# Performance work log

Measured on AMD Instinct MI355X. Metric: run time of the kernel, lower is better.

Reference implementation:

```python
import jax, jax.numpy as jnp
import numpy as np
import math

N = 1024
C = 128
H = 4
HD = C // H  # 32
HID = C // 2  # geom_mlp hidden


def setup_inputs() -> dict:
    key = jax.random.key(0)
    ks = jax.random.split(key, 12)
    s = 0.02
    return {
        "x": jax.random.normal(ks[0], (N, C), jnp.float32),
        "y": jax.random.normal(ks[1], (N, C), jnp.float32),
        "pos": jax.random.normal(ks[2], (N, 3), jnp.float32),
        "Wq": jax.random.normal(ks[3], (C, C), jnp.float32) * s,
        "bq": jnp.zeros((C,), jnp.float32),
        "Wk": jax.random.normal(ks[4], (C, C), jnp.float32) * s,
        "bk": jnp.zeros((C,), jnp.float32),
        "Wv": jax.random.normal(ks[5], (C, C), jnp.float32) * s,
        "bv": jnp.zeros((C,), jnp.float32),
        "W1": jax.random.normal(ks[6], (3, HID), jnp.float32) * s,
        "b1": jnp.zeros((HID,), jnp.float32),
        "W2": jax.random.normal(ks[7], (HID, C), jnp.float32) * s,
        "b2": jnp.zeros((C,), jnp.float32),
    }


def _safe_norm(sq):
    # sqrt with zero (sub)gradient at 0, matching torch.norm behavior
    pos_mask = sq > 0
    return jnp.where(pos_mask, jnp.sqrt(jnp.where(pos_mask, sq, 1.0)), 0.0)


def reference(x, y, pos, Wq, bq, Wk, bk, Wv, bv, W1, b1, W2, b2):
    # pairwise geometry
    pos_diff = pos[:, None, :] - pos[None, :, :]          # [N, N, 3]
    dist = _safe_norm(jnp.sum(pos_diff * pos_diff, -1))   # [N, N]
    geom = jax.nn.relu(pos_diff @ W1 + b1) @ W2 + b2      # [N, N, C]
    geom = geom.reshape(N, N, H, HD)                      # per-head split

    q = (x @ Wq + bq).reshape(N, H, HD)
    k = (y @ Wk + bk).reshape(N, H, HD)
    v = (y @ Wv + bv).reshape(N, H, HD)

    attn = jnp.einsum("ihd,jhd->hij", q, k) / math.sqrt(HD)  # [H, N, N]
    geom_attn = jnp.einsum("ihd,ijhd->hij", q, geom)         # [H, N, N]
    scores = attn + geom_attn - dist[None, :, :]
    p = jax.nn.softmax(scores, axis=-1)
    out = jnp.einsum("hij,jhd->ihd", p, v).reshape(N, C)     # [N, C]
    return out
```

## Files before the change

### kernel.cpp

```cpp
#include <hip/hip_runtime.h>
#include <math.h>


typedef float v2f __attribute__((ext_vector_type(2)));
typedef float v4f __attribute__((ext_vector_type(4)));

#define L2E 1.4426950408889634f
#define RSL (0.17677669529663687f * L2E)

static __device__ __forceinline__ float dot4(float4 a, float4 b) {
  return a.x*b.x + a.y*b.y + a.z*b.z + a.w*b.w;
}
static __device__ __forceinline__ v2f fma2(v2f a, v2f b, v2f c) {
  return __builtin_elementwise_fma(a, b, c);
}
static __device__ __forceinline__ v4f fma4s(float s, v4f b, v4f c) {
  v4f sv = {s, s, s, s};
  return __builtin_elementwise_fma(sv, b, c);
}
static __device__ __forceinline__ unsigned int bfr(float f) {
  unsigned int b = __float_as_uint(f);
  return (b + 0x7fffu + ((b >> 16) & 1u)) >> 16;
}
static __device__ __forceinline__ unsigned int pack2(float lo, float hi) {
  return bfr(lo) | (bfr(hi) << 16);
}
static __device__ __forceinline__ v2f unpk(unsigned int a) {
  v2f r;
  r.x = __uint_as_float(a << 16);
  r.y = __uint_as_float(a & 0xffff0000u);
  return r;
}

__global__ __launch_bounds__(384) void k_pre(
    const float* __restrict__ x, const float* __restrict__ y, const float* __restrict__ pos,
    const float* __restrict__ Wq, const float* __restrict__ bq,
    const float* __restrict__ Wk, const float* __restrict__ bk,
    const float* __restrict__ Wv, const float* __restrict__ bv,
    const float* __restrict__ W1, const float* __restrict__ b1,
    const float* __restrict__ W2, const float* __restrict__ b2,
    float* __restrict__ q, float* __restrict__ v,
    unsigned int* __restrict__ kTb, unsigned int* __restrict__ uTb,
    float* __restrict__ sA, float* __restrict__ pos4w)
{
  __shared__ float xs[256], ys[256], qs[256];
  __shared__ __align__(16) float4 W2S[64*33];

  const int t  = threadIdx.x;
  const int n0 = blockIdx.x * 2;

  if (t < 256) { xs[t] = x[n0*128 + t]; ys[t] = y[n0*128 + t]; }
  {
    const float4* w2g = (const float4*)W2;
    #pragma unroll
    for (int r = 0; r < 6; ++r) {
      const int e = t + 384*r;
      if (e < 2048) W2S[(e>>5)*33 + (e&31)] = w2g[e];
    }
  }
  __syncthreads();

  {
    const int c   = t & 127;
    const int mat = t >> 7;
    const float* W    = (mat == 0) ? Wq : (mat == 1 ? Wk : Wv);
    const float* S    = (mat == 0) ? xs : ys;
    const float* bias = (mat == 0) ? bq : (mat == 1 ? bk : bv);
    float a0 = 0.f, a1 = 0.f;
    #pragma unroll 8
    for (int d = 0; d < 128; ++d) {
      const float w_ = W[d*128 + c];
      a0 = fmaf(S[d],       w_, a0);
      a1 = fmaf(S[128 + d], w_, a1);
    }
    const float bb = bias[c];
    a0 += bb; a1 += bb;
    if (mat == 0) {
      q[n0*128 + c] = a0 * RSL; q[(n0+1)*128 + c] = a1 * RSL;
      qs[c] = a0; qs[128 + c] = a1;
    } else if (mat == 2) {
      v[n0*128 + c] = a0; v[(n0+1)*128 + c] = a1;
    } else {
      const float b0 = __shfl_xor(a0, 1);
      const float b1 = __shfl_xor(a1, 1);
      if ((c & 1) == 0) {
        const int idx = ((c>>2)*1024)*2 + ((c>>1)&1);
        kTb[idx + (n0  )*2] = pack2(a0, b0);
        kTb[idx + (n0+1)*2] = pack2(a1, b1);
      }
    }
  }
  __syncthreads();

  if (t < 256) {
    const int m = t & 63, h = t >> 6;
    const float4* qs4 = (const float4*)qs;
    #pragma unroll
    for (int ii = 0; ii < 2; ++ii) {
      float acc = 0.f;
      #pragma unroll
      for (int ch = 0; ch < 8; ++ch)
        acc += dot4(qs4[ii*32 + h*8 + ch], W2S[m*33 + h*8 + ch]);
      sA[(n0+ii)*328 + 8 + (m>>2)*20 + h*4 + (m&3)] = acc * L2E;
    }
    if (t < 8) {
      const int ii = t >> 2, h2 = t & 3;
      float ca = 0.f;
      #pragma unroll
      for (int d = 0; d < 32; ++d) ca = fmaf(qs[ii*128 + h2*32 + d], b2[h2*32 + d], ca);
      sA[(n0+ii)*328 + h2] = ca * L2E;
    } else if (t < 16) {
      const int tt = t-8, ii = tt>>2, cc = tt&3;
      sA[(n0+ii)*328 + 4 + cc] = (cc < 3) ? pos[(n0+ii)*3 + cc] * L2E : 0.f;
    } else if (t < 24) {
      const int tt = t-16, ii = tt>>2, cc = tt&3;
      pos4w[(n0+ii)*4 + cc] = (cc < 3) ? pos[(n0+ii)*3 + cc] * L2E : 0.f;
    }
  } else if (t < 320) {
    const int tt = t - 256, ii = tt >> 5, mp = tt & 31;
    const int m0 = mp * 2;
    float ua0 = 0.f, ua1 = 0.f;
    #pragma unroll
    for (int cc = 0; cc < 3; ++cc) {
      const float p = pos[(n0+ii)*3 + cc];
      ua0 = fmaf(p, W1[cc*64 + m0    ], ua0);
      ua1 = fmaf(p, W1[cc*64 + m0 + 1], ua1);
    }
    sA[(n0+ii)*328 + 8 + (m0>>2)*20 + 16 + (m0&3)    ] = ua0 + b1[m0];
    sA[(n0+ii)*328 + 8 + (m0>>2)*20 + 16 + (m0&3) + 1] = ua1 + b1[m0+1];
    uTb[((mp>>1)*1024 + (n0+ii))*2 + (mp&1)] = pack2(ua0, ua1);
  }
}

__global__ __launch_bounds__(1024, 8) void k_attn(
    const float* __restrict__ q, const float* __restrict__ v,
    const uint2* __restrict__ kTb, const uint2* __restrict__ uTb,
    const float* __restrict__ sA, const v4f* __restrict__ pos4,
    float* __restrict__ out)
{
  __shared__ __align__(16) float eL[16*544];
  __shared__ __align__(16) float rnum[8192];
  __shared__ float rden[128];

  const int t     = threadIdx.x;
  const int i0    = blockIdx.x * 2;
  const int w     = t >> 6;
  const int lane  = t & 63;
  const int c4    = lane & 31;
  const int rep   = lane >> 5;
  const int hh    = c4 >> 3;

  const int jb = w*64;
  const int j  = jb + lane;

  const float* sA0 = sA + i0*328;
  const float* sA1 = sA0 + 328;
  const float* q0  = q + i0*128;
  const float* q1  = q0 + 128;

  const float c00 = sA0[0], c01 = sA0[1], c02 = sA0[2], c03 = sA0[3];
  const float c10 = sA1[0], c11 = sA1[1], c12 = sA1[2], c13 = sA1[3];
  const float p0x = sA0[4], p0y = sA0[5], p0z = sA0[6];
  const float p1x = sA1[4], p1y = sA1[5], p1z = sA1[6];

  const v4f pj = pos4[j];
  const float d0x = p0x-pj.x, d0y = p0y-pj.y, d0z = p0z-pj.z;
  const float d1x = p1x-pj.x, d1y = p1y-pj.y, d1z = p1z-pj.z;
  const float dist0 = sqrtf(d0x*d0x + d0y*d0y + d0z*d0z);
  const float dist1 = sqrtf(d1x*d1x + d1y*d1y + d1z*d1z);

  v2f g0a={0.f,0.f}, g0b={0.f,0.f}, g0c={0.f,0.f}, g0d={0.f,0.f};
  v2f g1a={0.f,0.f}, g1b={0.f,0.f}, g1c={0.f,0.f}, g1d={0.f,0.f};
  #pragma unroll 4
  for (int mb = 0; mb < 16; ++mb) {
    const uint2 up_ = uTb[mb*1024 + j];
    const v2f uj01 = unpk(up_.x), uj23 = unpk(up_.y);
    const v2f z = {0.f, 0.f};
    {
      const float* ab = sA0 + 8 + mb*20;
      const v2f h01 = __builtin_elementwise_max(*(const v2f*)(ab+16) - uj01, z);
      const v2f h23 = __builtin_elementwise_max(*(const v2f*)(ab+18) - uj23, z);
      g0a = fma2(h01, *(const v2f*)(ab+ 0), g0a); g0a = fma2(h23, *(const v2f*)(ab+ 2), g0a);
      g0b = fma2(h01, *(const v2f*)(ab+ 4), g0b); g0b = fma2(h23, *(const v2f*)(ab+ 6), g0b);
      g0c = fma2(h01, *(const v2f*)(ab+ 8), g0c); g0c = fma2(h23, *(const v2f*)(ab+10), g0c);
      g0d = fma2(h01, *(const v2f*)(ab+12), g0d); g0d = fma2(h23, *(const v2f*)(ab+14), g0d);
    }
    {
      const float* ab = sA1 + 8 + mb*20;
      const v2f h01 = __builtin_elementwise_max(*(const v2f*)(ab+16) - uj01, z);
      const v2f h23 = __builtin_elementwise_max(*(const v2f*)(ab+18) - uj23, z);
      g1a = fma2(h01, *(const v2f*)(ab+ 0), g1a); g1a = fma2(h23, *(const v2f*)(ab+ 2), g1a);
      g1b = fma2(h01, *(const v2f*)(ab+ 4), g1b); g1b = fma2(h23, *(const v2f*)(ab+ 6), g1b);
      g1c = fma2(h01, *(const v2f*)(ab+ 8), g1c); g1c = fma2(h23, *(const v2f*)(ab+10), g1c);
      g1d = fma2(h01, *(const v2f*)(ab+12), g1d); g1d = fma2(h23, *(const v2f*)(ab+14), g1d);
    }
  }

  v2f s0a={0.f,0.f}, s0b={0.f,0.f}, s0c={0.f,0.f}, s0d={0.f,0.f};
  v2f s1a={0.f,0.f}, s1b={0.f,0.f}, s1c={0.f,0.f}, s1d={0.f,0.f};
  #pragma unroll 8
  for (int cb = 0; cb < 8; ++cb) {
    const uint2 kp0 = kTb[(cb     )*1024 + j];
    const uint2 kp1 = kTb[(cb +  8)*1024 + j];
    const uint2 kp2 = kTb[(cb + 16)*1024 + j];
    const uint2 kp3 = kTb[(cb + 24)*1024 + j];
    const v2f k0a = unpk(kp0.x), k0b = unpk(kp0.y);
    const v2f k1a = unpk(kp1.x), k1b = unpk(kp1.y);
    const v2f k2a = unpk(kp2.x), k2b = unpk(kp2.y);
    const v2f k3a = unpk(kp3.x), k3b = unpk(kp3.y);
    s0a = fma2(k0a, *(const v2f*)(q0 + cb*4      ), s0a); s0a = fma2(k0b, *(const v2f*)(q0 + cb*4 +  2), s0a);
    s0b = fma2(k1a, *(const v2f*)(q0 + cb*4 + 32 ), s0b); s0b = fma2(k1b, *(const v2f*)(q0 + cb*4 + 34), s0b);
    s0c = fma2(k2a, *(const v2f*)(q0 + cb*4 + 64 ), s0c); s0c = fma2(k2b, *(const v2f*)(q0 + cb*4 + 66), s0c);
    s0d = fma2(k3a, *(const v2f*)(q0 + cb*4 + 96 ), s0d); s0d = fma2(k3b, *(const v2f*)(q0 + cb*4 + 98), s0d);
    s1a = fma2(k0a, *(const v2f*)(q1 + cb*4      ), s1a); s1a = fma2(k0b, *(const v2f*)(q1 + cb*4 +  2), s1a);
    s1b = fma2(k1a, *(const v2f*)(q1 + cb*4 + 32 ), s1b); s1b = fma2(k1b, *(const v2f*)(q1 + cb*4 + 34), s1b);
    s1c = fma2(k2a, *(const v2f*)(q1 + cb*4 + 64 ), s1c); s1c = fma2(k2b, *(const v2f*)(q1 + cb*4 + 66), s1c);
    s1d = fma2(k3a, *(const v2f*)(q1 + cb*4 + 96 ), s1d); s1d = fma2(k3b, *(const v2f*)(q1 + cb*4 + 98), s1d);
  }

  float lsum[8];
  float* eW = &eL[w*544];
  {
    const v2f t0a = s0a + g0a, t0b = s0b + g0b, t0c = s0c + g0c, t0d = s0d + g0d;
    const float p0 = exp2f(t0a.x + t0a.y + (c00 - dist0));
    const float p1 = exp2f(t0b.x + t0b.y + (c01 - dist0));
    const float p2 = exp2f(t0c.x + t0c.y + (c02 - dist0));
    const float p3 = exp2f(t0d.x + t0d.y + (c03 - dist0));
    lsum[0] = p0; lsum[1] = p1; lsum[2] = p2; lsum[3] = p3;
    eW[      lane] = p0; eW[ 68 + lane] = p1; eW[136 + lane] = p2; eW[204 + lane] = p3;
    const v2f t1a = s1a + g1a, t1b = s1b + g1b, t1c = s1c + g1c, t1d = s1d + g1d;
    const float r0 = exp2f(t1a.x + t1a.y + (c10 - dist1));
    const float r1 = exp2f(t1b.x + t1b.y + (c11 - dist1));
    const float r2 = exp2f(t1c.x + t1c.y + (c12 - dist1));
    const float r3 = exp2f(t1d.x + t1d.y + (c13 - dist1));
    lsum[4] = r0; lsum[5] = r1; lsum[6] = r2; lsum[7] = r3;
    eW[272 + lane] = r0; eW[340 + lane] = r1; eW[408 + lane] = r2; eW[476 + lane] = r3;
  }
  __builtin_amdgcn_wave_barrier();

  v4f acc0 = {0.f,0.f,0.f,0.f};
  v4f acc1 = {0.f,0.f,0.f,0.f};
  {
    const v4f* er0 = (const v4f*)&eL[w*544 +  hh    *68 + rep*32];
    const v4f* er1 = (const v4f*)&eL[w*544 + (4+hh) *68 + rep*32];
    const v4f* vg = (const v4f*)(v + jb*128);
    const int vbase = rep*32*32 + c4;
    #pragma unroll 4
    for (int jj4 = 0; jj4 < 8; ++jj4) {
      const v4f e0 = er0[jj4];
      const v4f e1 = er1[jj4];
      const v4f va = vg[vbase + (jj4*4+0)*32];
      const v4f vb = vg[vbase + (jj4*4+1)*32];
      const v4f vc = vg[vbase + (jj4*4+2)*32];
      const v4f vd = vg[vbase + (jj4*4+3)*32];
      acc0 = fma4s(e0.x, va, acc0); acc1 = fma4s(e1.x, va, acc1);
      acc0 = fma4s(e0.y, vb, acc0); acc1 = fma4s(e1.y, vb, acc1);
      acc0 = fma4s(e0.z, vc, acc0); acc1 = fma4s(e1.z, vc, acc1);
      acc0 = fma4s(e0.w, vd, acc0); acc1 = fma4s(e1.w, vd, acc1);
    }
  }
  __builtin_amdgcn_wave_barrier();

  #pragma unroll
  for (int mm = 1; mm < 64; mm <<= 1) {
    #pragma unroll
    for (int r8 = 0; r8 < 8; ++r8) lsum[r8] += __shfl_xor(lsum[r8], mm);
  }
  ((v4f*)rnum)[((w*2+0)*2 + rep)*32 + c4] = acc0;
  ((v4f*)rnum)[((w*2+1)*2 + rep)*32 + c4] = acc1;
  if (lane == 0) {
    #pragma unroll
    for (int r8 = 0; r8 < 8; ++r8) rden[w*8 + r8] = lsum[r8];
  }
  __syncthreads();

  if (t < 256) {
    const int ii = t >> 7, c = t & 127;
    float num = 0.f, den = 0.f;
    #pragma unroll
    for (int ww = 0; ww < 16; ++ww) {
      num += rnum[((ww*2+ii)*2+0)*128 + c];
      num += rnum[((ww*2+ii)*2+1)*128 + c];
      den += rden[ww*8 + ii*4 + (c>>5)];
    }
    out[(i0+ii)*128 + c] = num / den;
  }
}

extern "C" void kernel_launch(void* const* d_in, const int* in_sizes, int n_in,
                              void* d_out, int out_size, void* d_ws, size_t ws_size,
                              hipStream_t stream) {
  const float* x   = (const float*)d_in[0];
  const float* y   = (const float*)d_in[1];
  const float* pos = (const float*)d_in[2];
  const float* Wq  = (const float*)d_in[3];
  const float* bq  = (const float*)d_in[4];
  const float* Wk  = (const float*)d_in[5];
  const float* bk  = (const float*)d_in[6];
  const float* Wv  = (const float*)d_in[7];
  const float* bv  = (const float*)d_in[8];
  const float* W1  = (const float*)d_in[9];
  const float* b1  = (const float*)d_in[10];
  const float* W2  = (const float*)d_in[11];
  const float* b2  = (const float*)d_in[12];

  float* ws = (float*)d_ws;
  float*        q    = ws;
  float*        v    = ws + 131072;
  unsigned int* kTb  = (unsigned int*)(ws + 262144);
  unsigned int* uTb  = (unsigned int*)(ws + 327680);
  float*        sA   = ws + 360448;
  float*        pos4 = ws + 696320;
  float*        out  = (float*)d_out;

  k_pre<<<dim3(512), dim3(384), 0, stream>>>(x, y, pos, Wq, bq, Wk, bk, Wv, bv,
                                             W1, b1, W2, b2,
                                             q, v, kTb, uTb, sA, pos4);
  k_attn<<<dim3(512), dim3(1024), 0, stream>>>(q, v, (const uint2*)kTb,
                                               (const uint2*)uTb, sA,
                                               (const v4f*)pos4, out);
}
```

Baseline: 116.9 us.

## Process four query rows per attention block to reuse K, U and V loads

Each k_attn block now handles four query rows instead of two, which halves the grid to 256 blocks. Every j-column load of uTb, kTb, pos4 and V is shared across four rows, so per-row global and L1 traffic is lower. Geometry and QK partial sums now go into a single accumulator set per row, and the lsum reduction is moved ahead of the PV loop. In exchange, register pressure and LDS usage double, launch bounds drop to four blocks per CU, and 256 blocks may underfill a 256-CU device.

```diff
diff --git a/kernel.cpp b/kernel.cpp
--- a/kernel.cpp
+++ b/kernel.cpp
@@ -132,18 +132,18 @@
   }
 }
 
-__global__ __launch_bounds__(1024, 8) void k_attn(
+__global__ __launch_bounds__(1024, 4) void k_attn(
     const float* __restrict__ q, const float* __restrict__ v,
     const uint2* __restrict__ kTb, const uint2* __restrict__ uTb,
     const float* __restrict__ sA, const v4f* __restrict__ pos4,
     float* __restrict__ out)
 {
-  __shared__ __align__(16) float eL[16*544];
-  __shared__ __align__(16) float rnum[8192];
-  __shared__ float rden[128];
+  __shared__ __align__(16) float eL[16*1088];
+  __shared__ __align__(16) float rnum[16384];
+  __shared__ float rden[256];
 
   const int t     = threadIdx.x;
-  const int i0    = blockIdx.x * 2;
+  const int i0    = blockIdx.x * 4;
   const int w     = t >> 6;
   const int lane  = t & 63;
   const int c4    = lane & 31;
@@ -155,50 +155,63 @@
 
   const float* sA0 = sA + i0*328;
   const float* sA1 = sA0 + 328;
+  const float* sA2 = sA0 + 656;
+  const float* sA3 = sA0 + 984;
   const float* q0  = q + i0*128;
   const float* q1  = q0 + 128;
+  const float* q2  = q0 + 256;
+  const float* q3  = q0 + 384;
 
   const float c00 = sA0[0], c01 = sA0[1], c02 = sA0[2], c03 = sA0[3];
   const float c10 = sA1[0], c11 = sA1[1], c12 = sA1[2], c13 = sA1[3];
+  const float c20 = sA2[0], c21 = sA2[1], c22 = sA2[2], c23 = sA2[3];
+  const float c30 = sA3[0], c31 = sA3[1], c32 = sA3[2], c33 = sA3[3];
   const float p0x = sA0[4], p0y = sA0[5], p0z = sA0[6];
   const float p1x = sA1[4], p1y = sA1[5], p1z = sA1[6];
+  const float p2x = sA2[4], p2y = sA2[5], p2z = sA2[6];
+  const float p3x = sA3[4], p3y = sA3[5], p3z = sA3[6];
 
   const v4f pj = pos4[j];
   const float d0x = p0x-pj.x, d0y = p0y-pj.y, d0z = p0z-pj.z;
   const float d1x = p1x-pj.x, d1y = p1y-pj.y, d1z = p1z-pj.z;
+  const float d2x = p2x-pj.x, d2y = p2y-pj.y, d2z = p2z-pj.z;
+  const float d3x = p3x-pj.x, d3y = p3y-pj.y, d3z = p3z-pj.z;
   const float dist0 = sqrtf(d0x*d0x + d0y*d0y + d0z*d0z);
   const float dist1 = sqrtf(d1x*d1x + d1y*d1y + d1z*d1z);
-
-  v2f g0a={0.f,0.f}, g0b={0.f,0.f}, g0c={0.f,0.f}, g0d={0.f,0.f};
-  v2f g1a={0.f,0.f}, g1b={0.f,0.f}, g1c={0.f,0.f}, g1d={0.f,0.f};
-  #pragma unroll 4
+  const float dist2 = sqrtf(d2x*d2x + d2y*d2y + d2z*d2z);
+  const float dist3 = sqrtf(d3x*d3x + d3y*d3y + d3z*d3z);
+
+  v2f s0a={0.f,0.f}, s0b={0.f,0.f}, s0c={0.f,0.f}, s0d={0.f,0.f};
+  v2f s1a={0.f,0.f}, s1b={0.f,0.f}, s1c={0.f,0.f}, s1d={0.f,0.f};
+  v2f s2a={0.f,0.f}, s2b={0.f,0.f}, s2c={0.f,0.f}, s2d={0.f,0.f};
+  v2f s3a={0.f,0.f}, s3b={0.f,0.f}, s3c={0.f,0.f}, s3d={0.f,0.f};
+  const v2f z = {0.f, 0.f};
+
+#define GEOM_ROW(r) { \
+    const float* ab = sA##r + 8 + mb*20; \
+    const v2f h01 = __builtin_elementwise_max(*(const v2f*)(ab+16) - uj01, z); \
+    const v2f h23 = __builtin_elementwise_max(*(const v2f*)(ab+18) - uj23, z); \
+    s##r##a = fma2(h01, *(const v2f*)(ab+ 0), s##r##a); s##r##a = fma2(h23, *(const v2f*)(ab+ 2), s##r##a); \
+    s##r##b = fma2(h01, *(const v2f*)(ab+ 4), s##r##b); s##r##b = fma2(h23, *(const v2f*)(ab+ 6), s##r##b); \
+    s##r##c = fma2(h01, *(const v2f*)(ab+ 8), s##r##c); s##r##c = fma2(h23, *(const v2f*)(ab+10), s##r##c); \
+    s##r##d = fma2(h01, *(const v2f*)(ab+12), s##r##d); s##r##d = fma2(h23, *(const v2f*)(ab+14), s##r##d); \
+  }
+  #pragma unroll 2
   for (int mb = 0; mb < 16; ++mb) {
     const uint2 up_ = uTb[mb*1024 + j];
     const v2f uj01 = unpk(up_.x), uj23 = unpk(up_.y);
-    const v2f z = {0.f, 0.f};
-    {
-      const float* ab = sA0 + 8 + mb*20;
-      const v2f h01 = __builtin_elementwise_max(*(const v2f*)(ab+16) - uj01, z);
-      const v2f h23 = __builtin_elementwise_max(*(const v2f*)(ab+18) - uj23, z);
-      g0a = fma2(h01, *(const v2f*)(ab+ 0), g0a); g0a = fma2(h23, *(const v2f*)(ab+ 2), g0a);
-      g0b = fma2(h01, *(const v2f*)(ab+ 4), g0b); g0b = fma2(h23, *(const v2f*)(ab+ 6), g0b);
-      g0c = fma2(h01, *(const v2f*)(ab+ 8), g0c); g0c = fma2(h23, *(const v2f*)(ab+10), g0c);
-      g0d = fma2(h01, *(const v2f*)(ab+12), g0d); g0d = fma2(h23, *(const v2f*)(ab+14), g0d);
-    }
-    {
-      const float* ab = sA1 + 8 + mb*20;
-      const v2f h01 = __builtin_elementwise_max(*(const v2f*)(ab+16) - uj01, z);
-      const v2f h23 = __builtin_elementwise_max(*(const v2f*)(ab+18) - uj23, z);
-      g1a = fma2(h01, *(const v2f*)(ab+ 0), g1a); g1a = fma2(h23, *(const v2f*)(ab+ 2), g1a);
-      g1b = fma2(h01, *(const v2f*)(ab+ 4), g1b); g1b = fma2(h23, *(const v2f*)(ab+ 6), g1b);
-      g1c = fma2(h01, *(const v2f*)(ab+ 8), g1c); g1c = fma2(h23, *(const v2f*)(ab+10), g1c);
-      g1d = fma2(h01, *(const v2f*)(ab+12), g1d); g1d = fma2(h23, *(const v2f*)(ab+14), g1d);
-    }
-  }
-
-  v2f s0a={0.f,0.f}, s0b={0.f,0.f}, s0c={0.f,0.f}, s0d={0.f,0.f};
-  v2f s1a={0.f,0.f}, s1b={0.f,0.f}, s1c={0.f,0.f}, s1d={0.f,0.f};
-  #pragma unroll 8
+    GEOM_ROW(0) GEOM_ROW(1) GEOM_ROW(2) GEOM_ROW(3)
+  }
+#undef GEOM_ROW
+
+#define QK_ROW(r) { \
+    const float* qq = q##r + cb*4; \
+    s##r##a = fma2(k0a, *(const v2f*)(qq      ), s##r##a); s##r##a = fma2(k0b, *(const v2f*)(qq +  2), s##r##a); \
+    s##r##b = fma2(k1a, *(const v2f*)(qq + 32 ), s##r##b); s##r##b = fma2(k1b, *(const v2f*)(qq + 34), s##r##b); \
+    s##r##c = fma2(k2a, *(const v2f*)(qq + 64 ), s##r##c); s##r##c = fma2(k2b, *(const v2f*)(qq + 66), s##r##c); \
+    s##r##d = fma2(k3a, *(const v2f*)(qq + 96 ), s##r##d); s##r##d = fma2(k3b, *(const v2f*)(qq + 98), s##r##d); \
+  }
+  #pragma unroll 2
   for (int cb = 0; cb < 8; ++cb) {
     const uint2 kp0 = kTb[(cb     )*1024 + j];
     const uint2 kp1 = kTb[(cb +  8)*1024 + j];
@@ -208,80 +221,85 @@
     const v2f k1a = unpk(kp1.x), k1b = unpk(kp1.y);
     const v2f k2a = unpk(kp2.x), k2b = unpk(kp2.y);
     const v2f k3a = unpk(kp3.x), k3b = unpk(kp3.y);
-    s0a = fma2(k0a, *(const v2f*)(q0 + cb*4      ), s0a); s0a = fma2(k0b, *(const v2f*)(q0 + cb*4 +  2), s0a);
-    s0b = fma2(k1a, *(const v2f*)(q0 + cb*4 + 32 ), s0b); s0b = fma2(k1b, *(const v2f*)(q0 + cb*4 + 34), s0b);
-    s0c = fma2(k2a, *(const v2f*)(q0 + cb*4 + 64 ), s0c); s0c = fma2(k2b, *(const v2f*)(q0 + cb*4 + 66), s0c);
-    s0d = fma2(k3a, *(const v2f*)(q0 + cb*4 + 96 ), s0d); s0d = fma2(k3b, *(const v2f*)(q0 + cb*4 + 98), s0d);
-    s1a = fma2(k0a, *(const v2f*)(q1 + cb*4      ), s1a); s1a = fma2(k0b, *(const v2f*)(q1 + cb*4 +  2), s1a);
-    s1b = fma2(k1a, *(const v2f*)(q1 + cb*4 + 32 ), s1b); s1b = fma2(k1b, *(const v2f*)(q1 + cb*4 + 34), s1b);
-    s1c = fma2(k2a, *(const v2f*)(q1 + cb*4 + 64 ), s1c); s1c = fma2(k2b, *(const v2f*)(q1 + cb*4 + 66), s1c);
-    s1d = fma2(k3a, *(const v2f*)(q1 + cb*4 + 96 ), s1d); s1d = fma2(k3b, *(const v2f*)(q1 + cb*4 + 98), s1d);
-  }
-
-  float lsum[8];
-  float* eW = &eL[w*544];
-  {
-    const v2f t0a = s0a + g0a, t0b = s0b + g0b, t0c = s0c + g0c, t0d = s0d + g0d;
-    const float p0 = exp2f(t0a.x + t0a.y + (c00 - dist0));
-    const float p1 = exp2f(t0b.x + t0b.y + (c01 - dist0));
-    const float p2 = exp2f(t0c.x + t0c.y + (c02 - dist0));
-    const float p3 = exp2f(t0d.x + t0d.y + (c03 - dist0));
-    lsum[0] = p0; lsum[1] = p1; lsum[2] = p2; lsum[3] = p3;
-    eW[      lane] = p0; eW[ 68 + lane] = p1; eW[136 + lane] = p2; eW[204 + lane] = p3;
-    const v2f t1a = s1a + g1a, t1b = s1b + g1b, t1c = s1c + g1c, t1d = s1d + g1d;
-    const float r0 = exp2f(t1a.x + t1a.y + (c10 - dist1));
-    const float r1 = exp2f(t1b.x + t1b.y + (c11 - dist1));
-    const float r2 = exp2f(t1c.x + t1c.y + (c12 - dist1));
-    const float r3 = exp2f(t1d.x + t1d.y + (c13 - dist1));
-    lsum[4] = r0; lsum[5] = r1; lsum[6] = r2; lsum[7] = r3;
-    eW[272 + lane] = r0; eW[340 + lane] = r1; eW[408 + lane] = r2; eW[476 + lane] = r3;
-  }
+    QK_ROW(0) QK_ROW(1) QK_ROW(2) QK_ROW(3)
+  }
+#undef QK_ROW
+
+  float lsum[16];
+  float* eW = &eL[w*1088];
+#define EXP_ROW(r, C0, C1, C2, C3, DIST) { \
+    const float p0 = exp2f(s##r##a.x + s##r##a.y + (C0 - DIST)); \
+    const float p1 = exp2f(s##r##b.x + s##r##b.y + (C1 - DIST)); \
+    const float p2 = exp2f(s##r##c.x + s##r##c.y + (C2 - DIST)); \
+    const float p3 = exp2f(s##r##d.x + s##r##d.y + (C3 - DIST)); \
+    lsum[r*4+0] = p0; lsum[r*4+1] = p1; lsum[r*4+2] = p2; lsum[r*4+3] = p3; \
+    eW[(r*4+0)*68 + lane] = p0; eW[(r*4+1)*68 + lane] = p1; \
+    eW[(r*4+2)*68 + lane] = p2; eW[(r*4+3)*68 + lane] = p3; \
+  }
+  EXP_ROW(0, c00, c01, c02, c03, dist0)
+  EXP_ROW(1, c10, c11, c12, c13, dist1)
+  EXP_ROW(2, c20, c21, c22, c23, dist2)
+  EXP_ROW(3, c30, c31, c32, c33, dist3)
+#undef EXP_ROW
   __builtin_amdgcn_wave_barrier();
+
+  #pragma unroll
+  for (int mm = 1; mm < 64; mm <<= 1) {
+    #pragma unroll
+    for (int r16 = 0; r16 < 16; ++r16) lsum[r16] += __shfl_xor(lsum[r16], mm);
+  }
+  if (lane == 0) {
+    #pragma unroll
+    for (int r16 = 0; r16 < 16; ++r16) rden[w*16 + r16] = lsum[r16];
+  }
 
   v4f acc0 = {0.f,0.f,0.f,0.f};
   v4f acc1 = {0.f,0.f,0.f,0.f};
+  v4f acc2 = {0.f,0.f,0.f,0.f};
+  v4f acc3 = {0.f,0.f,0.f,0.f};
   {
-    const v4f* er0 = (const v4f*)&eL[w*544 +  hh    *68 + rep*32];
-    const v4f* er1 = (const v4f*)&eL[w*544 + (4+hh) *68 + rep*32];
+    const v4f* er0 = (const v4f*)&eL[w*1088 + ( 0 + hh)*68 + rep*32];
+    const v4f* er1 = (const v4f*)&eL[w*1088 + ( 4 + hh)*68 + rep*32];
+    const v4f* er2 = (const v4f*)&eL[w*1088 + ( 8 + hh)*68 + rep*32];
+    const v4f* er3 = (const v4f*)&eL[w*1088 + (12 + hh)*68 + rep*32];
     const v4f* vg = (const v4f*)(v + jb*128);
     const int vbase = rep*32*32 + c4;
-    #pragma unroll 4
+    #pragma unroll 2
     for (int jj4 = 0; jj4 < 8; ++jj4) {
       const v4f e0 = er0[jj4];
       const v4f e1 = er1[jj4];
+      const v4f e2 = er2[jj4];
+      const v4f e3 = er3[jj4];
       const v4f va = vg[vbase + (jj4*4+0)*32];
       const v4f vb = vg[vbase + (jj4*4+1)*32];
       const v4f vc = vg[vbase + (jj4*4+2)*32];
       const v4f vd = vg[vbase + (jj4*4+3)*32];
       acc0 = fma4s(e0.x, va, acc0); acc1 = fma4s(e1.x, va, acc1);
+      acc2 = fma4s(e2.x, va, acc2); acc3 = fma4s(e3.x, va, acc3);
       acc0 = fma4s(e0.y, vb, acc0); acc1 = fma4s(e1.y, vb, acc1);
+      acc2 = fma4s(e2.y, vb, acc2); acc3 = fma4s(e3.y, vb, acc3);
       acc0 = fma4s(e0.z, vc, acc0); acc1 = fma4s(e1.z, vc, acc1);
+      acc2 = fma4s(e2.z, vc, acc2); acc3 = fma4s(e3.z, vc, acc3);
       acc0 = fma4s(e0.w, vd, acc0); acc1 = fma4s(e1.w, vd, acc1);
+      acc2 = fma4s(e2.w, vd, acc2); acc3 = fma4s(e3.w, vd, acc3);
     }
   }
   __builtin_amdgcn_wave_barrier();
 
-  #pragma unroll
-  for (int mm = 1; mm < 64; mm <<= 1) {
-    #pragma unroll
-    for (int r8 = 0; r8 < 8; ++r8) lsum[r8] += __shfl_xor(lsum[r8], mm);
-  }
-  ((v4f*)rnum)[((w*2+0)*2 + rep)*32 + c4] = acc0;
-  ((v4f*)rnum)[((w*2+1)*2 + rep)*32 + c4] = acc1;
-  if (lane == 0) {
-    #pragma unroll
-    for (int r8 = 0; r8 < 8; ++r8) rden[w*8 + r8] = lsum[r8];
-  }
+  ((v4f*)rnum)[((w*4+0)*2 + rep)*32 + c4] = acc0;
+  ((v4f*)rnum)[((w*4+1)*2 + rep)*32 + c4] = acc1;
+  ((v4f*)rnum)[((w*4+2)*2 + rep)*32 + c4] = acc2;
+  ((v4f*)rnum)[((w*4+3)*2 + rep)*32 + c4] = acc3;
   __syncthreads();
 
-  if (t < 256) {
+  if (t < 512) {
     const int ii = t >> 7, c = t & 127;
     float num = 0.f, den = 0.f;
     #pragma unroll
     for (int ww = 0; ww < 16; ++ww) {
-      num += rnum[((ww*2+ii)*2+0)*128 + c];
-      num += rnum[((ww*2+ii)*2+1)*128 + c];
-      den += rden[ww*8 + ii*4 + (c>>5)];
+      num += rnum[((ww*4+ii)*2+0)*128 + c];
+      num += rnum[((ww*4+ii)*2+1)*128 + c];
+      den += rden[ww*16 + ii*4 + (c>>5)];
     }
     out[(i0+ii)*128 + c] = num / den;
   }
@@ -316,7 +334,7 @@
   k_pre<<<dim3(512), dim3(384), 0, stream>>>(x, y, pos, Wq, bq, Wk, bk, Wv, bv,
                                              W1, b1, W2, b2,
                                              q, v, kTb, uTb, sA, pos4);
-  k_attn<<<dim3(512), dim3(1024), 0, stream>>>(q, v, (const uint2*)kTb,
+  k_attn<<<dim3(256), dim3(1024), 0, stream>>>(q, v, (const uint2*)kTb,
                                                (const uint2*)uTb, sA,
                                                (const v4f*)pos4, out);
 }
```

Measured after the change: 120.4 us. +3.0%, slower.

## Switch QK and PV products to packed fp16 dot2 with repacked layouts

Applied to the files above, without the earlier changes.

Stores q, k and v as packed fp16 pairs in new layouts (k as 8-word rows, v interleaved across j pairs, u widened to 4-word loads) and computes both the QK scores and the P·V accumulation with v_dot2 fp16 instructions. Probabilities are rounded to fp16, packed two per word in LDS, and the denominator is built from the same rounded values so it stays consistent with the numerator. This halves LDS and global traffic for e and v and reduces the FMA count. In exchange it loses precision (fp16 range and rounding for q, k, v and p) and adds extra shuffles for packing.

```diff
diff --git a/kernel.cpp b/kernel.cpp
--- a/kernel.cpp
+++ b/kernel.cpp
@@ -1,9 +1,11 @@
 #include <hip/hip_runtime.h>
+#include <hip/hip_fp16.h>
 #include <math.h>
 
 
 typedef float v2f __attribute__((ext_vector_type(2)));
 typedef float v4f __attribute__((ext_vector_type(4)));
+typedef __fp16 h2f __attribute__((ext_vector_type(2)));
 
 #define L2E 1.4426950408889634f
 #define RSL (0.17677669529663687f * L2E)
@@ -13,10 +15,6 @@
 }
 static __device__ __forceinline__ v2f fma2(v2f a, v2f b, v2f c) {
   return __builtin_elementwise_fma(a, b, c);
-}
-static __device__ __forceinline__ v4f fma4s(float s, v4f b, v4f c) {
-  v4f sv = {s, s, s, s};
-  return __builtin_elementwise_fma(sv, b, c);
 }
 static __device__ __forceinline__ unsigned int bfr(float f) {
   unsigned int b = __float_as_uint(f);
@@ -30,6 +28,24 @@
   r.x = __uint_as_float(a << 16);
   r.y = __uint_as_float(a & 0xffff0000u);
   return r;
+}
+static __device__ __forceinline__ unsigned int pkh(float lo, float hi) {
+  h2f r = __builtin_amdgcn_cvt_pkrtz(lo, hi);
+  return __builtin_bit_cast(unsigned int, r);
+}
+static __device__ __forceinline__ unsigned int pkrn(float lo, float hi) {
+  unsigned int a = (unsigned int)__half_as_ushort(__float2half(lo));
+  unsigned int b = (unsigned int)__half_as_ushort(__float2half(hi));
+  return a | (b << 16);
+}
+static __device__ __forceinline__ float fdot2h(unsigned int a_, unsigned int b_, float acc) {
+  return __builtin_amdgcn_fdot2(__builtin_bit_cast(h2f, a_),
+                                __builtin_bit_cast(h2f, b_), acc, false);
+}
+static __device__ __forceinline__ float r2h(float x, unsigned int* bits) {
+  h2f t = __builtin_amdgcn_cvt_pkrtz(x, x);
+  *bits = __builtin_bit_cast(unsigned int, t) & 0xffffu;
+  return (float)t.x;
 }
 
 __global__ __launch_bounds__(384) void k_pre(
@@ -39,8 +55,8 @@
     const float* __restrict__ Wv, const float* __restrict__ bv,
     const float* __restrict__ W1, const float* __restrict__ b1,
     const float* __restrict__ W2, const float* __restrict__ b2,
-    float* __restrict__ q, float* __restrict__ v,
-    unsigned int* __restrict__ kTb, unsigned int* __restrict__ uTb,
+    unsigned int* __restrict__ qT, unsigned int* __restrict__ vJ,
+    unsigned int* __restrict__ kT8, unsigned int* __restrict__ uT4,
     float* __restrict__ sA, float* __restrict__ pos4w)
 {
   __shared__ float xs[256], ys[256], qs[256];
@@ -76,17 +92,24 @@
     const float bb = bias[c];
     a0 += bb; a1 += bb;
     if (mat == 0) {
-      q[n0*128 + c] = a0 * RSL; q[(n0+1)*128 + c] = a1 * RSL;
       qs[c] = a0; qs[128 + c] = a1;
+      const float sa0 = a0 * RSL, sa1 = a1 * RSL;
+      const float tb0 = __shfl_xor(sa0, 1);
+      const float tb1 = __shfl_xor(sa1, 1);
+      if ((c & 1) == 0) {
+        qT[(n0  )*64 + (c>>1)] = pkh(sa0, tb0);
+        qT[(n0+1)*64 + (c>>1)] = pkh(sa1, tb1);
+      }
     } else if (mat == 2) {
-      v[n0*128 + c] = a0; v[(n0+1)*128 + c] = a1;
+      vJ[(n0>>1)*128 + c] = pkrn(a0, a1);
     } else {
       const float b0 = __shfl_xor(a0, 1);
       const float b1 = __shfl_xor(a1, 1);
       if ((c & 1) == 0) {
-        const int idx = ((c>>2)*1024)*2 + ((c>>1)&1);
-        kTb[idx + (n0  )*2] = pack2(a0, b0);
-        kTb[idx + (n0+1)*2] = pack2(a1, b1);
+        const int qi = c >> 2, cbv = qi & 7, slot = qi >> 3, wrd = (c >> 1) & 1;
+        const int base = (cbv*1024 + n0)*8 + slot*2 + wrd;
+        kT8[base]     = pkh(a0, b0);
+        kT8[base + 8] = pkh(a1, b1);
       }
     }
   }
@@ -128,17 +151,17 @@
     }
     sA[(n0+ii)*328 + 8 + (m0>>2)*20 + 16 + (m0&3)    ] = ua0 + b1[m0];
     sA[(n0+ii)*328 + 8 + (m0>>2)*20 + 16 + (m0&3) + 1] = ua1 + b1[m0+1];
-    uTb[((mp>>1)*1024 + (n0+ii))*2 + (mp&1)] = pack2(ua0, ua1);
+    uT4[((mp>>2)*1024 + (n0+ii))*4 + (mp&3)] = pack2(ua0, ua1);
   }
 }
 
 __global__ __launch_bounds__(1024, 8) void k_attn(
-    const float* __restrict__ q, const float* __restrict__ v,
-    const uint2* __restrict__ kTb, const uint2* __restrict__ uTb,
+    const unsigned int* __restrict__ qT, const unsigned int* __restrict__ vJ,
+    const unsigned int* __restrict__ kT8, const unsigned int* __restrict__ uT4,
     const float* __restrict__ sA, const v4f* __restrict__ pos4,
     float* __restrict__ out)
 {
-  __shared__ __align__(16) float eL[16*544];
+  __shared__ __align__(16) unsigned int eL16[16*272];
   __shared__ __align__(16) float rnum[8192];
   __shared__ float rden[128];
 
@@ -155,8 +178,6 @@
 
   const float* sA0 = sA + i0*328;
   const float* sA1 = sA0 + 328;
-  const float* q0  = q + i0*128;
-  const float* q1  = q0 + 128;
 
   const float c00 = sA0[0], c01 = sA0[1], c02 = sA0[2], c03 = sA0[3];
   const float c10 = sA1[0], c11 = sA1[1], c12 = sA1[2], c13 = sA1[3];
@@ -171,107 +192,115 @@
 
   v2f g0a={0.f,0.f}, g0b={0.f,0.f}, g0c={0.f,0.f}, g0d={0.f,0.f};
   v2f g1a={0.f,0.f}, g1b={0.f,0.f}, g1c={0.f,0.f}, g1d={0.f,0.f};
-  #pragma unroll 4
-  for (int mb = 0; mb < 16; ++mb) {
-    const uint2 up_ = uTb[mb*1024 + j];
-    const v2f uj01 = unpk(up_.x), uj23 = unpk(up_.y);
-    const v2f z = {0.f, 0.f};
-    {
-      const float* ab = sA0 + 8 + mb*20;
-      const v2f h01 = __builtin_elementwise_max(*(const v2f*)(ab+16) - uj01, z);
-      const v2f h23 = __builtin_elementwise_max(*(const v2f*)(ab+18) - uj23, z);
-      g0a = fma2(h01, *(const v2f*)(ab+ 0), g0a); g0a = fma2(h23, *(const v2f*)(ab+ 2), g0a);
-      g0b = fma2(h01, *(const v2f*)(ab+ 4), g0b); g0b = fma2(h23, *(const v2f*)(ab+ 6), g0b);
-      g0c = fma2(h01, *(const v2f*)(ab+ 8), g0c); g0c = fma2(h23, *(const v2f*)(ab+10), g0c);
-      g0d = fma2(h01, *(const v2f*)(ab+12), g0d); g0d = fma2(h23, *(const v2f*)(ab+14), g0d);
-    }
-    {
-      const float* ab = sA1 + 8 + mb*20;
-      const v2f h01 = __builtin_elementwise_max(*(const v2f*)(ab+16) - uj01, z);
-      const v2f h23 = __builtin_elementwise_max(*(const v2f*)(ab+18) - uj23, z);
-      g1a = fma2(h01, *(const v2f*)(ab+ 0), g1a); g1a = fma2(h23, *(const v2f*)(ab+ 2), g1a);
-      g1b = fma2(h01, *(const v2f*)(ab+ 4), g1b); g1b = fma2(h23, *(const v2f*)(ab+ 6), g1b);
-      g1c = fma2(h01, *(const v2f*)(ab+ 8), g1c); g1c = fma2(h23, *(const v2f*)(ab+10), g1c);
-      g1d = fma2(h01, *(const v2f*)(ab+12), g1d); g1d = fma2(h23, *(const v2f*)(ab+14), g1d);
-    }
-  }
-
-  v2f s0a={0.f,0.f}, s0b={0.f,0.f}, s0c={0.f,0.f}, s0d={0.f,0.f};
-  v2f s1a={0.f,0.f}, s1b={0.f,0.f}, s1c={0.f,0.f}, s1d={0.f,0.f};
-  #pragma unroll 8
-  for (int cb = 0; cb < 8; ++cb) {
-    const uint2 kp0 = kTb[(cb     )*1024 + j];
-    const uint2 kp1 = kTb[(cb +  8)*1024 + j];
-    const uint2 kp2 = kTb[(cb + 16)*1024 + j];
-    const uint2 kp3 = kTb[(cb + 24)*1024 + j];
-    const v2f k0a = unpk(kp0.x), k0b = unpk(kp0.y);
-    const v2f k1a = unpk(kp1.x), k1b = unpk(kp1.y);
-    const v2f k2a = unpk(kp2.x), k2b = unpk(kp2.y);
-    const v2f k3a = unpk(kp3.x), k3b = unpk(kp3.y);
-    s0a = fma2(k0a, *(const v2f*)(q0 + cb*4      ), s0a); s0a = fma2(k0b, *(const v2f*)(q0 + cb*4 +  2), s0a);
-    s0b = fma2(k1a, *(const v2f*)(q0 + cb*4 + 32 ), s0b); s0b = fma2(k1b, *(const v2f*)(q0 + cb*4 + 34), s0b);
-    s0c = fma2(k2a, *(const v2f*)(q0 + cb*4 + 64 ), s0c); s0c = fma2(k2b, *(const v2f*)(q0 + cb*4 + 66), s0c);
-    s0d = fma2(k3a, *(const v2f*)(q0 + cb*4 + 96 ), s0d); s0d = fma2(k3b, *(const v2f*)(q0 + cb*4 + 98), s0d);
-    s1a = fma2(k0a, *(const v2f*)(q1 + cb*4      ), s1a); s1a = fma2(k0b, *(const v2f*)(q1 + cb*4 +  2), s1a);
-    s1b = fma2(k1a, *(const v2f*)(q1 + cb*4 + 32 ), s1b); s1b = fma2(k1b, *(const v2f*)(q1 + cb*4 + 34), s1b);
-    s1c = fma2(k2a, *(const v2f*)(q1 + cb*4 + 64 ), s1c); s1c = fma2(k2b, *(const v2f*)(q1 + cb*4 + 66), s1c);
-    s1d = fma2(k3a, *(const v2f*)(q1 + cb*4 + 96 ), s1d); s1d = fma2(k3b, *(const v2f*)(q1 + cb*4 + 98), s1d);
+  {
+    const uint4* ug = (const uint4*)uT4;
+#define GEOM_MB(MB, W01, W23) { \
+    const v2f uj01 = unpk(W01), uj23 = unpk(W23); \
+    const v2f z = {0.f, 0.f}; \
+    { \
+      const float* ab = sA0 + 8 + (MB)*20; \
+      const v2f h01 = __builtin_elementwise_max(*(const v2f*)(ab+16) - uj01, z); \
+      const v2f h23 = __builtin_elementwise_max(*(const v2f*)(ab+18) - uj23, z); \
+      g0a = fma2(h01, *(const v2f*)(ab+ 0), g0a); g0a = fma2(h23, *(const v2f*)(ab+ 2), g0a); \
+      g0b = fma2(h01, *(const v2f*)(ab+ 4), g0b); g0b = fma2(h23, *(const v2f*)(ab+ 6), g0b); \
+      g0c = fma2(h01, *(const v2f*)(ab+ 8), g0c); g0c = fma2(h23, *(const v2f*)(ab+10), g0c); \
+      g0d = fma2(h01, *(const v2f*)(ab+12), g0d); g0d = fma2(h23, *(const v2f*)(ab+14), g0d); \
+    } \
+    { \
+      const float* ab = sA1 + 8 + (MB)*20; \
+      const v2f h01 = __builtin_elementwise_max(*(const v2f*)(ab+16) - uj01, z); \
+      const v2f h23 = __builtin_elementwise_max(*(const v2f*)(ab+18) - uj23, z); \
+      g1a = fma2(h01, *(const v2f*)(ab+ 0), g1a); g1a = fma2(h23, *(const v2f*)(ab+ 2), g1a); \
+      g1b = fma2(h01, *(const v2f*)(ab+ 4), g1b); g1b = fma2(h23, *(const v2f*)(ab+ 6), g1b); \
+      g1c = fma2(h01, *(const v2f*)(ab+ 8), g1c); g1c = fma2(h23, *(const v2f*)(ab+10), g1c); \
+      g1d = fma2(h01, *(const v2f*)(ab+12), g1d); g1d = fma2(h23, *(const v2f*)(ab+14), g1d); \
+    } \
+  }
+    #pragma unroll 2
+    for (int g = 0; g < 8; ++g) {
+      const uint4 uw = ug[g*1024 + j];
+      GEOM_MB(2*g,     uw.x, uw.y)
+      GEOM_MB(2*g + 1, uw.z, uw.w)
+    }
+#undef GEOM_MB
+  }
+
+  float t0a = g0a.x + g0a.y, t0b = g0b.x + g0b.y;
+  float t0c = g0c.x + g0c.y, t0d = g0d.x + g0d.y;
+  float t1a = g1a.x + g1a.y, t1b = g1b.x + g1b.y;
+  float t1c = g1c.x + g1c.y, t1d = g1d.x + g1d.y;
+
+  {
+    const uint4* kg = (const uint4*)kT8;
+    const unsigned int* qT0 = qT + i0*64;
+    const unsigned int* qT1 = qT0 + 64;
+    #pragma unroll 8
+    for (int cb = 0; cb < 8; ++cb) {
+      const uint4 ka = kg[(cb*1024 + j)*2];
+      const uint4 kb = kg[(cb*1024 + j)*2 + 1];
+      t0a = fdot2h(ka.x, qT0[     cb*2], t0a); t0a = fdot2h(ka.y, qT0[     cb*2+1], t0a);
+      t0b = fdot2h(ka.z, qT0[16 + cb*2], t0b); t0b = fdot2h(ka.w, qT0[16 + cb*2+1], t0b);
+      t0c = fdot2h(kb.x, qT0[32 + cb*2], t0c); t0c = fdot2h(kb.y, qT0[32 + cb*2+1], t0c);
+      t0d = fdot2h(kb.z, qT0[48 + cb*2], t0d); t0d = fdot2h(kb.w, qT0[48 + cb*2+1], t0d);
+      t1a = fdot2h(ka.x, qT1[     cb*2], t1a); t1a = fdot2h(ka.y, qT1[     cb*2+1], t1a);
+      t1b = fdot2h(ka.z, qT1[16 + cb*2], t1b); t1b = fdot2h(ka.w, qT1[16 + cb*2+1], t1b);
+      t1c = fdot2h(kb.x, qT1[32 + cb*2], t1c); t1c = fdot2h(kb.y, qT1[32 + cb*2+1], t1c);
+      t1d = fdot2h(kb.z, qT1[48 + cb*2], t1d); t1d = fdot2h(kb.w, qT1[48 + cb*2+1], t1d);
+    }
   }
 
   float lsum[8];
-  float* eW = &eL[w*544];
-  {
-    const v2f t0a = s0a + g0a, t0b = s0b + g0b, t0c = s0c + g0c, t0d = s0d + g0d;
-    const float p0 = exp2f(t0a.x + t0a.y + (c00 - dist0));
-    const float p1 = exp2f(t0b.x + t0b.y + (c01 - dist0));
-    const float p2 = exp2f(t0c.x + t0c.y + (c02 - dist0));
-    const float p3 = exp2f(t0d.x + t0d.y + (c03 - dist0));
-    lsum[0] = p0; lsum[1] = p1; lsum[2] = p2; lsum[3] = p3;
-    eW[      lane] = p0; eW[ 68 + lane] = p1; eW[136 + lane] = p2; eW[204 + lane] = p3;
-    const v2f t1a = s1a + g1a, t1b = s1b + g1b, t1c = s1c + g1c, t1d = s1d + g1d;
-    const float r0 = exp2f(t1a.x + t1a.y + (c10 - dist1));
-    const float r1 = exp2f(t1b.x + t1b.y + (c11 - dist1));
-    const float r2 = exp2f(t1c.x + t1c.y + (c12 - dist1));
-    const float r3 = exp2f(t1d.x + t1d.y + (c13 - dist1));
-    lsum[4] = r0; lsum[5] = r1; lsum[6] = r2; lsum[7] = r3;
-    eW[272 + lane] = r0; eW[340 + lane] = r1; eW[408 + lane] = r2; eW[476 + lane] = r3;
+  unsigned int eb[8];
+  lsum[0] = r2h(exp2f(t0a + (c00 - dist0)), &eb[0]);
+  lsum[1] = r2h(exp2f(t0b + (c01 - dist0)), &eb[1]);
+  lsum[2] = r2h(exp2f(t0c + (c02 - dist0)), &eb[2]);
+  lsum[3] = r2h(exp2f(t0d + (c03 - dist0)), &eb[3]);
+  lsum[4] = r2h(exp2f(t1a + (c10 - dist1)), &eb[4]);
+  lsum[5] = r2h(exp2f(t1b + (c11 - dist1)), &eb[5]);
+  lsum[6] = r2h(exp2f(t1c + (c12 - dist1)), &eb[6]);
+  lsum[7] = r2h(exp2f(t1d + (c13 - dist1)), &eb[7]);
+  {
+    unsigned int* eW = &eL16[w*272];
+    const int jp = lane >> 1;
+    #pragma unroll
+    for (int r8 = 0; r8 < 8; ++r8) {
+      const unsigned int pb = __shfl_xor(eb[r8], 1);
+      if ((lane & 1) == 0) eW[r8*34 + jp] = eb[r8] | (pb << 16);
+    }
   }
   __builtin_amdgcn_wave_barrier();
+
+  #pragma unroll
+  for (int mm = 1; mm < 64; mm <<= 1) {
+    #pragma unroll
+    for (int r8 = 0; r8 < 8; ++r8) lsum[r8] += __shfl_xor(lsum[r8], mm);
+  }
+  if (lane == 0) {
+    #pragma unroll
+    for (int r8 = 0; r8 < 8; ++r8) rden[w*8 + r8] = lsum[r8];
+  }
 
   v4f acc0 = {0.f,0.f,0.f,0.f};
   v4f acc1 = {0.f,0.f,0.f,0.f};
   {
-    const v4f* er0 = (const v4f*)&eL[w*544 +  hh    *68 + rep*32];
-    const v4f* er1 = (const v4f*)&eL[w*544 + (4+hh) *68 + rep*32];
-    const v4f* vg = (const v4f*)(v + jb*128);
-    const int vbase = rep*32*32 + c4;
+    const unsigned int* eW0 = &eL16[w*272 +  hh   *34 + rep*16];
+    const unsigned int* eW1 = &eL16[w*272 + (4+hh)*34 + rep*16];
+    const uint4* vg = (const uint4*)vJ + (w*32 + rep*16)*32 + c4;
     #pragma unroll 4
-    for (int jj4 = 0; jj4 < 8; ++jj4) {
-      const v4f e0 = er0[jj4];
-      const v4f e1 = er1[jj4];
-      const v4f va = vg[vbase + (jj4*4+0)*32];
-      const v4f vb = vg[vbase + (jj4*4+1)*32];
-      const v4f vc = vg[vbase + (jj4*4+2)*32];
-      const v4f vd = vg[vbase + (jj4*4+3)*32];
-      acc0 = fma4s(e0.x, va, acc0); acc1 = fma4s(e1.x, va, acc1);
-      acc0 = fma4s(e0.y, vb, acc0); acc1 = fma4s(e1.y, vb, acc1);
-      acc0 = fma4s(e0.z, vc, acc0); acc1 = fma4s(e1.z, vc, acc1);
-      acc0 = fma4s(e0.w, vd, acc0); acc1 = fma4s(e1.w, vd, acc1);
+    for (int m = 0; m < 16; ++m) {
+      const uint4 vw = vg[m*32];
+      const unsigned int e0 = eW0[m];
+      const unsigned int e1 = eW1[m];
+      acc0.x = fdot2h(vw.x, e0, acc0.x); acc0.y = fdot2h(vw.y, e0, acc0.y);
+      acc0.z = fdot2h(vw.z, e0, acc0.z); acc0.w = fdot2h(vw.w, e0, acc0.w);
+      acc1.x = fdot2h(vw.x, e1, acc1.x); acc1.y = fdot2h(vw.y, e1, acc1.y);
+      acc1.z = fdot2h(vw.z, e1, acc1.z); acc1.w = fdot2h(vw.w, e1, acc1.w);
     }
   }
   __builtin_amdgcn_wave_barrier();
 
-  #pragma unroll
-  for (int mm = 1; mm < 64; mm <<= 1) {
-    #pragma unroll
-    for (int r8 = 0; r8 < 8; ++r8) lsum[r8] += __shfl_xor(lsum[r8], mm);
-  }
   ((v4f*)rnum)[((w*2+0)*2 + rep)*32 + c4] = acc0;
   ((v4f*)rnum)[((w*2+1)*2 + rep)*32 + c4] = acc1;
-  if (lane == 0) {
-    #pragma unroll
-    for (int r8 = 0; r8 < 8; ++r8) rden[w*8 + r8] = lsum[r8];
-  }
   __syncthreads();
 
   if (t < 256) {
@@ -305,18 +334,17 @@
   const float* b2  = (const float*)d_in[12];
 
   float* ws = (float*)d_ws;
-  float*        q    = ws;
-  float*        v    = ws + 131072;
-  unsigned int* kTb  = (unsigned int*)(ws + 262144);
-  unsigned int* uTb  = (unsigned int*)(ws + 327680);
+  unsigned int* qT   = (unsigned int*)ws;
+  unsigned int* vJ   = (unsigned int*)(ws + 131072);
+  unsigned int* kT8  = (unsigned int*)(ws + 262144);
+  unsigned int* uT4  = (unsigned int*)(ws + 327680);
   float*        sA   = ws + 360448;
   float*        pos4 = ws + 696320;
   float*        out  = (float*)d_out;
 
   k_pre<<<dim3(512), dim3(384), 0, stream>>>(x, y, pos, Wq, bq, Wk, bk, Wv, bv,
                                              W1, b1, W2, b2,
-                                             q, v, kTb, uTb, sA, pos4);
-  k_attn<<<dim3(512), dim3(1024), 0, stream>>>(q, v, (const uint2*)kTb,
-                                               (const uint2*)uTb, sA,
+                                             qT, vJ, kT8, uT4, sA, pos4);
+  k_attn<<<dim3(512), dim3(1024), 0, stream>>>(qT, vJ, kT8, uT4, sA,
                                                (const v4f*)pos4, out);
 }
```

Result: slower. 158.6 us (+35.7%).
